# Kernel tuning notes

Measured on AMD Instinct MI355X. Metric: run time of the kernel, lower is better.

Reference implementation:

```python
import jax, jax.numpy as jnp
import numpy as np
from jax.ops import segment_sum

N_NODES = 100000
N_EDGES = 1600000
N_GRAPHS = 2048
VOCAB = 1000
EMBED = 64
HID = 64
N_CL = 2


def setup_inputs() -> dict:
    key = jax.random.key(0)
    ks = jax.random.split(key, 9)
    x = jax.random.randint(ks[0], (N_NODES,), 0, VOCAB)
    edge_index = jax.random.randint(ks[1], (2, N_EDGES), 0, N_NODES)
    batch = jnp.sort(jax.random.randint(ks[2], (N_NODES,), 0, N_GRAPHS))
    emb = jax.random.normal(ks[3], (VOCAB, EMBED), dtype=jnp.float32)
    emb = emb.at[0].set(0.0)  # padding_idx=0
    s1 = 1.0 / np.sqrt(EMBED)
    s2 = 1.0 / np.sqrt(HID)
    W1 = jax.random.uniform(ks[4], (EMBED, HID), jnp.float32, -s1, s1)
    b1 = jnp.zeros((HID,), jnp.float32)
    W2 = jax.random.uniform(ks[5], (HID, HID), jnp.float32, -s2, s2)
    b2 = jnp.zeros((HID,), jnp.float32)
    Wl = jax.random.uniform(ks[6], (HID, N_CL), jnp.float32, -s2, s2)
    bl = jax.random.uniform(ks[7], (N_CL,), jnp.float32, -s2, s2)
    return {"x": x, "edge_index": edge_index, "batch": batch,
            "emb": emb, "W1": W1, "b1": b1, "W2": W2, "b2": b2,
            "Wl": Wl, "bl": bl}


def _gcn_conv(h, row, col, norm, W, b):
    # h: [N, Fin] -> [N, Fout]; PyG GCNConv: lin -> gather -> norm -> scatter-add -> bias
    h = h @ W
    msg = h[row] * norm[:, None]          # [E+N, Fout] gathered, normalized messages
    out = segment_sum(msg, col, num_segments=N_NODES)
    return out + b


def reference(x, edge_index, batch, emb, W1, b1, W2, b2, Wl, bl):
    # add self loops (GCNConv default)
    loop = jnp.arange(N_NODES)
    row = jnp.concatenate([edge_index[0], loop])  # sources
    col = jnp.concatenate([edge_index[1], loop])  # targets
    # symmetric normalization: deg^{-1/2}[row] * deg^{-1/2}[col]
    deg = segment_sum(jnp.ones_like(col, dtype=jnp.float32), col, num_segments=N_NODES)
    dinv = jnp.where(deg > 0, jax.lax.rsqrt(jnp.maximum(deg, 1.0)), 0.0)
    norm = dinv[row] * dinv[col]

    h = emb[x]                                        # [N, EMBED]
    h = jax.nn.relu(_gcn_conv(h, row, col, norm, W1, b1))
    h = jax.nn.relu(_gcn_conv(h, row, col, norm, W2, b2))

    # global mean pool over graphs
    sums = segment_sum(h, batch, num_segments=N_GRAPHS)          # [G, HID]
    cnts = segment_sum(jnp.ones((N_NODES,), jnp.float32), batch, num_segments=N_GRAPHS)
    pooled = sums / jnp.maximum(cnts, 1.0)[:, None]
    return pooled @ Wl + bl                                      # [G, N_CL]
```

## Files before the change

kernel.cpp:

```cpp
#include <hip/hip_runtime.h>
#include <hip/hip_bf16.h>

#define N_NODES  100000
#define N_EDGES  1600000
#define N_GRAPHS 2048
#define VOCAB    1000
#define EMBED    64
#define HID      64
#define N_CL     2
#define CAP      64
#define NBLK     391
#define EBLK     6250
#define VBLK     63
#define NSWEEP   8
#define RANGE    12500

typedef __hip_bfloat162 bf2;

__device__ inline uint2 pack_bf16x4(float4 a) {
    bf2 lo = __float22bfloat162_rn(make_float2(a.x, a.y));
    bf2 hi = __float22bfloat162_rn(make_float2(a.z, a.w));
    uint2 r;
    r.x = *reinterpret_cast<unsigned*>(&lo);
    r.y = *reinterpret_cast<unsigned*>(&hi);
    return r;
}

__device__ inline void acc_bf16x8(float4& a, float4& b, uint4 raw) {
    bf2 p0 = *reinterpret_cast<bf2*>(&raw.x);
    bf2 p1 = *reinterpret_cast<bf2*>(&raw.y);
    bf2 p2 = *reinterpret_cast<bf2*>(&raw.z);
    bf2 p3 = *reinterpret_cast<bf2*>(&raw.w);
    float2 f0 = __bfloat1622float2(p0);
    float2 f1 = __bfloat1622float2(p1);
    float2 f2 = __bfloat1622float2(p2);
    float2 f3 = __bfloat1622float2(p3);
    a.x += f0.x; a.y += f0.y; a.z += f1.x; a.w += f1.y;
    b.x += f2.x; b.y += f2.y; b.z += f3.x; b.w += f3.y;
}

__device__ inline void xor_reduce8(float4& A, float4& B) {
#pragma unroll
    for (int m = 8; m <= 32; m <<= 1) {
        A.x += __shfl_xor(A.x, m, 64); A.y += __shfl_xor(A.y, m, 64);
        A.z += __shfl_xor(A.z, m, 64); A.w += __shfl_xor(A.w, m, 64);
        B.x += __shfl_xor(B.x, m, 64); B.y += __shfl_xor(B.y, m, 64);
        B.z += __shfl_xor(B.z, m, 64); B.w += __shfl_xor(B.w, m, 64);
    }
}

__global__ __launch_bounds__(256) void k_fill_slots(const int* __restrict__ row, const int* __restrict__ col,
                                                    int* __restrict__ cnt, int* __restrict__ slots,
                                                    const int* __restrict__ batch, int* __restrict__ start,
                                                    const float* __restrict__ emb, const float* __restrict__ W1,
                                                    float* __restrict__ E) {
    int bid = blockIdx.x;
    if (bid < NSWEEP * EBLK) {
        int sweep = bid & (NSWEEP - 1);
        int e = (bid >> 3) * 256 + threadIdx.x;
        int c = col[e];
        if ((unsigned)(c - sweep * RANGE) < (unsigned)RANGE) {
            int pos = atomicAdd(&cnt[c], 1);
            if (pos < CAP) slots[c * CAP + pos] = row[e];
        }
    } else if (bid < NSWEEP * EBLK + NBLK) {
        int v = (bid - NSWEEP * EBLK) * 256 + threadIdx.x;
        if (v >= N_NODES) return;
        int b = batch[v];
        int pb = (v == 0) ? -1 : batch[v - 1];
        for (int g = pb + 1; g <= b; ++g) start[g] = v;
        if (v == N_NODES - 1)
            for (int g = b + 1; g <= N_GRAPHS; ++g) start[g] = N_NODES;
    } else {
        int t = (bid - NSWEEP * EBLK - NBLK) * 256 + threadIdx.x;
        int j = t >> 4;
        int f4 = t & 15;
        if (j >= VOCAB) return;
        const float4* W4 = (const float4*)W1;
        const float* er = emb + j * EMBED;
        float4 acc = make_float4(0.f, 0.f, 0.f, 0.f);
#pragma unroll 8
        for (int k = 0; k < EMBED; ++k) {
            float hv = er[k];
            float4 w = W4[k * 16 + f4];
            acc.x += hv * w.x; acc.y += hv * w.y; acc.z += hv * w.z; acc.w += hv * w.w;
        }
        ((float4*)E)[t] = acc;
    }
}

__global__ __launch_bounds__(256) void k_tn1(const int* __restrict__ x, const int* __restrict__ cnt,
                                             const float* __restrict__ E, uint2* __restrict__ tn) {
    int t = blockIdx.x * 256 + threadIdx.x;
    int v = t >> 4;
    int f4 = t & 15;
    float d = rsqrtf((float)(cnt[v] + 1));
    float4 a = ((const float4*)E)[x[v] * 16 + f4];
    a.x *= d; a.y *= d; a.z *= d; a.w *= d;
    tn[t] = pack_bf16x4(a);
}

__global__ __launch_bounds__(256) void k_agg_gemm(const uint4* __restrict__ tn,
                                                  const int* __restrict__ cnt,
                                                  const int* __restrict__ slots,
                                                  const float* __restrict__ bias,
                                                  const float* __restrict__ W2,
                                                  __hip_bfloat16* __restrict__ tn2) {
    __shared__ float hrow[8][HID];
    int wid = threadIdx.x >> 6;
    int lane = threadIdx.x & 63;
    int fg = lane & 7;
    int es = lane >> 3;
    int v0 = blockIdx.x * 8 + wid * 2;
    int v1 = v0 + 1;
    int c0 = cnt[v0], c1 = cnt[v1];
    int n0 = min(c0, CAP), n1 = min(c1, CAP);
    const int* sl0 = slots + v0 * CAP;
    const int* sl1 = slots + v1 * CAP;
    float4 a0A = make_float4(0.f, 0.f, 0.f, 0.f), a0B = a0A, a1A = a0A, a1B = a0A;
    if (es == 0) acc_bf16x8(a0A, a0B, tn[v0 * 8 + fg]);
    if (es == 1) acc_bf16x8(a1A, a1B, tn[v1 * 8 + fg]);
    int m = max(n0, n1);
    int i = 0;
    for (; i + 16 <= m; i += 16) {
        int ia = i + es, ib = i + 8 + es;
        if (ia < n0) { uint4 r = tn[sl0[ia] * 8 + fg]; acc_bf16x8(a0A, a0B, r); }
        if (ia < n1) { uint4 r = tn[sl1[ia] * 8 + fg]; acc_bf16x8(a1A, a1B, r); }
        if (ib < n0) { uint4 r = tn[sl0[ib] * 8 + fg]; acc_bf16x8(a0A, a0B, r); }
        if (ib < n1) { uint4 r = tn[sl1[ib] * 8 + fg]; acc_bf16x8(a1A, a1B, r); }
    }
    for (; i < m; i += 8) {
        int ia = i + es;
        if (ia < n0) { uint4 r = tn[sl0[ia] * 8 + fg]; acc_bf16x8(a0A, a0B, r); }
        if (ia < n1) { uint4 r = tn[sl1[ia] * 8 + fg]; acc_bf16x8(a1A, a1B, r); }
    }
    xor_reduce8(a0A, a0B);
    xor_reduce8(a1A, a1B);
    float d0 = rsqrtf((float)(c0 + 1));
    float d1 = rsqrtf((float)(c1 + 1));
    float4 bA = ((const float4*)bias)[fg * 2 + 0];
    float4 bB = ((const float4*)bias)[fg * 2 + 1];
    if (es == 0) {
        float4 oA, oB;
        oA.x = fmaxf(d0 * a0A.x + bA.x, 0.f); oA.y = fmaxf(d0 * a0A.y + bA.y, 0.f);
        oA.z = fmaxf(d0 * a0A.z + bA.z, 0.f); oA.w = fmaxf(d0 * a0A.w + bA.w, 0.f);
        oB.x = fmaxf(d0 * a0B.x + bB.x, 0.f); oB.y = fmaxf(d0 * a0B.y + bB.y, 0.f);
        oB.z = fmaxf(d0 * a0B.z + bB.z, 0.f); oB.w = fmaxf(d0 * a0B.w + bB.w, 0.f);
        ((float4*)&hrow[wid * 2][fg * 8])[0] = oA;
        ((float4*)&hrow[wid * 2][fg * 8])[1] = oB;
    }
    if (es == 1) {
        float4 oA, oB;
        oA.x = fmaxf(d1 * a1A.x + bA.x, 0.f); oA.y = fmaxf(d1 * a1A.y + bA.y, 0.f);
        oA.z = fmaxf(d1 * a1A.z + bA.z, 0.f); oA.w = fmaxf(d1 * a1A.w + bA.w, 0.f);
        oB.x = fmaxf(d1 * a1B.x + bB.x, 0.f); oB.y = fmaxf(d1 * a1B.y + bB.y, 0.f);
        oB.z = fmaxf(d1 * a1B.z + bB.z, 0.f); oB.w = fmaxf(d1 * a1B.w + bB.w, 0.f);
        ((float4*)&hrow[wid * 2 + 1][fg * 8])[0] = oA;
        ((float4*)&hrow[wid * 2 + 1][fg * 8])[1] = oB;
    }
    __syncthreads();
    const float* hr0 = hrow[wid * 2];
    const float* hr1 = hrow[wid * 2 + 1];
    float s0 = 0.f, s1 = 0.f;
#pragma unroll 8
    for (int k = 0; k < HID; ++k) {
        float w = W2[k * HID + lane];
        s0 += hr0[k] * w;
        s1 += hr1[k] * w;
    }
    tn2[v0 * HID + lane] = __float2bfloat16(d0 * s0);
    tn2[v1 * HID + lane] = __float2bfloat16(d1 * s1);
}

__global__ __launch_bounds__(256) void k_agg(const uint4* __restrict__ tn,
                                             const int* __restrict__ cnt,
                                             const int* __restrict__ slots,
                                             const float* __restrict__ bias,
                                             float* __restrict__ h) {
    int wid = threadIdx.x >> 6;
    int lane = threadIdx.x & 63;
    int fg = lane & 7;
    int es = lane >> 3;
    int v0 = blockIdx.x * 8 + wid * 2;
    int v1 = v0 + 1;
    int c0 = cnt[v0], c1 = cnt[v1];
    int n0 = min(c0, CAP), n1 = min(c1, CAP);
    const int* sl0 = slots + v0 * CAP;
    const int* sl1 = slots + v1 * CAP;
    float4 a0A = make_float4(0.f, 0.f, 0.f, 0.f), a0B = a0A, a1A = a0A, a1B = a0A;
    if (es == 0) acc_bf16x8(a0A, a0B, tn[v0 * 8 + fg]);
    if (es == 1) acc_bf16x8(a1A, a1B, tn[v1 * 8 + fg]);
    int m = max(n0, n1);
    int i = 0;
    for (; i + 16 <= m; i += 16) {
        int ia = i + es, ib = i + 8 + es;
        if (ia < n0) { uint4 r = tn[sl0[ia] * 8 + fg]; acc_bf16x8(a0A, a0B, r); }
        if (ia < n1) { uint4 r = tn[sl1[ia] * 8 + fg]; acc_bf16x8(a1A, a1B, r); }
        if (ib < n0) { uint4 r = tn[sl0[ib] * 8 + fg]; acc_bf16x8(a0A, a0B, r); }
        if (ib < n1) { uint4 r = tn[sl1[ib] * 8 + fg]; acc_bf16x8(a1A, a1B, r); }
    }
    for (; i < m; i += 8) {
        int ia = i + es;
        if (ia < n0) { uint4 r = tn[sl0[ia] * 8 + fg]; acc_bf16x8(a0A, a0B, r); }
        if (ia < n1) { uint4 r = tn[sl1[ia] * 8 + fg]; acc_bf16x8(a1A, a1B, r); }
    }
    xor_reduce8(a0A, a0B);
    xor_reduce8(a1A, a1B);
    float4 bA = ((const float4*)bias)[fg * 2 + 0];
    float4 bB = ((const float4*)bias)[fg * 2 + 1];
    if (es == 0) {
        float d0 = rsqrtf((float)(c0 + 1));
        float4 oA, oB;
        oA.x = fmaxf(d0 * a0A.x + bA.x, 0.f); oA.y = fmaxf(d0 * a0A.y + bA.y, 0.f);
        oA.z = fmaxf(d0 * a0A.z + bA.z, 0.f); oA.w = fmaxf(d0 * a0A.w + bA.w, 0.f);
        oB.x = fmaxf(d0 * a0B.x + bB.x, 0.f); oB.y = fmaxf(d0 * a0B.y + bB.y, 0.f);
        oB.z = fmaxf(d0 * a0B.z + bB.z, 0.f); oB.w = fmaxf(d0 * a0B.w + bB.w, 0.f);
        ((float4*)&h[v0 * HID + fg * 8])[0] = oA;
        ((float4*)&h[v0 * HID + fg * 8])[1] = oB;
    }
    if (es == 1) {
        float d1 = rsqrtf((float)(c1 + 1));
        float4 oA, oB;
        oA.x = fmaxf(d1 * a1A.x + bA.x, 0.f); oA.y = fmaxf(d1 * a1A.y + bA.y, 0.f);
        oA.z = fmaxf(d1 * a1A.z + bA.z, 0.f); oA.w = fmaxf(d1 * a1A.w + bA.w, 0.f);
        oB.x = fmaxf(d1 * a1B.x + bB.x, 0.f); oB.y = fmaxf(d1 * a1B.y + bB.y, 0.f);
        oB.z = fmaxf(d1 * a1B.z + bB.z, 0.f); oB.w = fmaxf(d1 * a1B.w + bB.w, 0.f);
        ((float4*)&h[v1 * HID + fg * 8])[0] = oA;
        ((float4*)&h[v1 * HID + fg * 8])[1] = oB;
    }
}

__global__ __launch_bounds__(256) void k_pool_out(const float* __restrict__ h,
                                                  const int* __restrict__ start,
                                                  const float* __restrict__ Wl,
                                                  const float* __restrict__ bl,
                                                  float* __restrict__ out) {
    int g = (blockIdx.x * 256 + threadIdx.x) >> 6;
    int f = threadIdx.x & 63;
    if (g >= N_GRAPHS) return;
    int s = start[g], e = start[g + 1];
    float acc = 0.f;
    int v = s;
    for (; v + 4 <= e; v += 4) {
        float a0 = h[(v + 0) * HID + f];
        float a1 = h[(v + 1) * HID + f];
        float a2 = h[(v + 2) * HID + f];
        float a3 = h[(v + 3) * HID + f];
        acc += (a0 + a1) + (a2 + a3);
    }
    for (; v < e; ++v) acc += h[v * HID + f];
    float m = acc / fmaxf((float)(e - s), 1.f);
    float p0 = m * Wl[f * N_CL + 0];
    float p1 = m * Wl[f * N_CL + 1];
#pragma unroll
    for (int off = 32; off > 0; off >>= 1) {
        p0 += __shfl_down(p0, off, 64);
        p1 += __shfl_down(p1, off, 64);
    }
    if (f == 0) {
        out[g * N_CL + 0] = p0 + bl[0];
        out[g * N_CL + 1] = p1 + bl[1];
    }
}

extern "C" void kernel_launch(void* const* d_in, const int* in_sizes, int n_in,
                              void* d_out, int out_size, void* d_ws, size_t ws_size,
                              hipStream_t stream) {
    const int*   x     = (const int*)d_in[0];
    const int*   ei    = (const int*)d_in[1];
    const int*   batch = (const int*)d_in[2];
    const float* emb   = (const float*)d_in[3];
    const float* W1    = (const float*)d_in[4];
    const float* b1    = (const float*)d_in[5];
    const float* W2    = (const float*)d_in[6];
    const float* b2    = (const float*)d_in[7];
    const float* Wl    = (const float*)d_in[8];
    const float* bl    = (const float*)d_in[9];
    float* out = (float*)d_out;

    const int* row = ei;
    const int* col = ei + N_EDGES;

    char* ws = (char*)d_ws;
    size_t off = 0;
    auto alloc = [&](size_t bytes) { char* p = ws + off; off = (off + bytes + 511) & ~(size_t)511; return p; };
    const size_t FEAT_BYTES  = (size_t)N_NODES * HID * sizeof(float);
    const size_t FEATB_BYTES = (size_t)N_NODES * HID * sizeof(__hip_bfloat16);
    float* A      = (float*)alloc(FEAT_BYTES);
    __hip_bfloat16* Bt = (__hip_bfloat16*)alloc(FEATB_BYTES);
    int*   slots  = (int*)  alloc((size_t)N_NODES * CAP * sizeof(int));
    float* E      = (float*)alloc((size_t)VOCAB * HID * sizeof(float));
    int*   start  = (int*)  alloc((size_t)(N_GRAPHS + 1) * sizeof(int));
    int*   cnt    = (int*)  alloc((size_t)N_NODES * sizeof(int));

    dim3 blk(256);
    dim3 g_fill(NSWEEP * EBLK + NBLK + VBLK);
    dim3 g_tn1(N_NODES * 16 / 256);
    dim3 g_agg(N_NODES / 8);
    dim3 g_po((N_GRAPHS * 64 + 255) / 256);

    hipMemsetAsync(cnt, 0, (size_t)N_NODES * sizeof(int), stream);

    k_fill_slots<<<g_fill, blk, 0, stream>>>(row, col, cnt, slots, batch, start, emb, W1, E);

    k_tn1<<<g_tn1, blk, 0, stream>>>(x, cnt, E, (uint2*)A);

    k_agg_gemm<<<g_agg, blk, 0, stream>>>((const uint4*)A, cnt, slots, b1, W2, Bt);

    k_agg<<<g_agg, blk, 0, stream>>>((const uint4*)Bt, cnt, slots, b2, A);

    k_pool_out<<<g_po, blk, 0, stream>>>(A, start, Wl, bl, out);
}
```

Measured before the change: 272.2 us.

## Pre-partition edges by target range before slot fill

```diff
diff --git a/kernel.cpp b/kernel.cpp
--- a/kernel.cpp
+++ b/kernel.cpp
@@ -10,10 +10,13 @@
 #define N_CL     2
 #define CAP      64
 #define NBLK     391
-#define EBLK     6250
 #define VBLK     63
 #define NSWEEP   8
 #define RANGE    12500
+#define ABLK     1563
+#define LCAP     320
+#define PCAP     225024
+#define PBLK     879
 
 typedef __hip_bfloat162 bf2;
 
@@ -49,22 +52,49 @@
     }
 }
 
-__global__ __launch_bounds__(256) void k_fill_slots(const int* __restrict__ row, const int* __restrict__ col,
-                                                    int* __restrict__ cnt, int* __restrict__ slots,
-                                                    const int* __restrict__ batch, int* __restrict__ start,
-                                                    const float* __restrict__ emb, const float* __restrict__ W1,
-                                                    float* __restrict__ E) {
+__global__ __launch_bounds__(256) void k_partition(const int* __restrict__ row, const int* __restrict__ col,
+                                                   int* __restrict__ partCnt, unsigned* __restrict__ part,
+                                                   const int* __restrict__ batch, int* __restrict__ start,
+                                                   const float* __restrict__ emb, const float* __restrict__ W1,
+                                                   float* __restrict__ E) {
     int bid = blockIdx.x;
-    if (bid < NSWEEP * EBLK) {
-        int sweep = bid & (NSWEEP - 1);
-        int e = (bid >> 3) * 256 + threadIdx.x;
-        int c = col[e];
-        if ((unsigned)(c - sweep * RANGE) < (unsigned)RANGE) {
-            int pos = atomicAdd(&cnt[c], 1);
-            if (pos < CAP) slots[c * CAP + pos] = row[e];
+    if (bid < ABLK) {
+        __shared__ unsigned buf[NSWEEP][LCAP];
+        __shared__ int lcnt[NSWEEP];
+        __shared__ int base[NSWEEP];
+        if (threadIdx.x < NSWEEP) lcnt[threadIdx.x] = 0;
+        __syncthreads();
+        int e0 = bid * 1024 + threadIdx.x;
+#pragma unroll
+        for (int j = 0; j < 4; ++j) {
+            int e = e0 + j * 256;
+            if (e < N_EDGES) {
+                int c = col[e];
+                int s = c / RANGE;
+                unsigned p = ((unsigned)row[e] << 14) | (unsigned)(c - s * RANGE);
+                int pos = atomicAdd(&lcnt[s], 1);
+                if (pos < LCAP) buf[s][pos] = p;
+                else {
+                    int gp = atomicAdd(&partCnt[s * 16], 1);
+                    part[s * PCAP + gp] = p;
+                }
+            }
         }
-    } else if (bid < NSWEEP * EBLK + NBLK) {
-        int v = (bid - NSWEEP * EBLK) * 256 + threadIdx.x;
+        __syncthreads();
+        if (threadIdx.x < NSWEEP) {
+            int n = min(lcnt[threadIdx.x], LCAP);
+            base[threadIdx.x] = atomicAdd(&partCnt[threadIdx.x * 16], n);
+        }
+        __syncthreads();
+#pragma unroll
+        for (int s = 0; s < NSWEEP; ++s) {
+            int n = min(lcnt[s], LCAP);
+            int b = base[s];
+            for (int t = threadIdx.x; t < n; t += 256)
+                part[s * PCAP + b + t] = buf[s][t];
+        }
+    } else if (bid < ABLK + NBLK) {
+        int v = (bid - ABLK) * 256 + threadIdx.x;
         if (v >= N_NODES) return;
         int b = batch[v];
         int pb = (v == 0) ? -1 : batch[v - 1];
@@ -72,7 +102,7 @@
         if (v == N_NODES - 1)
             for (int g = b + 1; g <= N_GRAPHS; ++g) start[g] = N_NODES;
     } else {
-        int t = (bid - NSWEEP * EBLK - NBLK) * 256 + threadIdx.x;
+        int t = (bid - ABLK - NBLK) * 256 + threadIdx.x;
         int j = t >> 4;
         int f4 = t & 15;
         if (j >= VOCAB) return;
@@ -87,6 +117,19 @@
         }
         ((float4*)E)[t] = acc;
     }
+}
+
+__global__ __launch_bounds__(256) void k_fill2(const int* __restrict__ partCnt, const unsigned* __restrict__ part,
+                                               int* __restrict__ cnt, int* __restrict__ slots) {
+    int bid = blockIdx.x;
+    int sweep = bid & (NSWEEP - 1);
+    int idx = (bid >> 3) * 256 + threadIdx.x;
+    if (idx >= partCnt[sweep * 16]) return;
+    unsigned p = part[sweep * PCAP + idx];
+    int c = sweep * RANGE + (int)(p & 16383u);
+    int r = (int)(p >> 14);
+    int pos = atomicAdd(&cnt[c], 1);
+    if (pos < CAP) slots[c * CAP + pos] = r;
 }
 
 __global__ __launch_bounds__(256) void k_tn1(const int* __restrict__ x, const int* __restrict__ cnt,
@@ -289,19 +332,24 @@
     float* A      = (float*)alloc(FEAT_BYTES);
     __hip_bfloat16* Bt = (__hip_bfloat16*)alloc(FEATB_BYTES);
     int*   slots  = (int*)  alloc((size_t)N_NODES * CAP * sizeof(int));
+    unsigned* part= (unsigned*)alloc((size_t)NSWEEP * PCAP * sizeof(unsigned));
     float* E      = (float*)alloc((size_t)VOCAB * HID * sizeof(float));
     int*   start  = (int*)  alloc((size_t)(N_GRAPHS + 1) * sizeof(int));
     int*   cnt    = (int*)  alloc((size_t)N_NODES * sizeof(int));
+    int*   partCnt= (int*)  alloc((size_t)NSWEEP * 16 * sizeof(int));
 
     dim3 blk(256);
-    dim3 g_fill(NSWEEP * EBLK + NBLK + VBLK);
+    dim3 g_part(ABLK + NBLK + VBLK);
+    dim3 g_fill2(NSWEEP * PBLK);
     dim3 g_tn1(N_NODES * 16 / 256);
     dim3 g_agg(N_NODES / 8);
     dim3 g_po((N_GRAPHS * 64 + 255) / 256);
 
-    hipMemsetAsync(cnt, 0, (size_t)N_NODES * sizeof(int), stream);
-
-    k_fill_slots<<<g_fill, blk, 0, stream>>>(row, col, cnt, slots, batch, start, emb, W1, E);
+    hipMemsetAsync(cnt, 0, (size_t)N_NODES * sizeof(int) + (size_t)NSWEEP * 16 * sizeof(int) + 512, stream);
+
+    k_partition<<<g_part, blk, 0, stream>>>(row, col, partCnt, part, batch, start, emb, W1, E);
+
+    k_fill2<<<g_fill2, blk, 0, stream>>>(partCnt, part, cnt, slots);
 
     k_tn1<<<g_tn1, blk, 0, stream>>>(x, cnt, E, (uint2*)A);
 
```

Measured after the change: 302.7 us. 11.2% more time.
